# Performance work log

Measured on AMD Instinct MI355X. Metric: run time of the kernel, lower is better.

## Reference

```python
import jax, jax.numpy as jnp
import numpy as np

N = 50000          # nodes
E = 800000         # edges (avg degree 16)
NFEAT = 128        # dim_touched / gcn_nfeat
NHID = 96
NCLASS = 64
EXTRA = 32         # extra MLP-only features
NHID1, NHID2 = 128, 64
NN = 70            # top-k threshold rank
EPS = 1e-5         # BatchNorm1d eps


def setup_inputs() -> dict:
    key = jax.random.key(0)
    ks = jax.random.split(key, 24)
    x = jax.random.normal(ks[0], (N, NFEAT + EXTRA + 1), jnp.float32)
    grp = jax.random.randint(ks[1], (N,), 0, 2).astype(jnp.float32)
    x = x.at[:, -1].set(grp)  # last column is the group flag (target_group == 0)
    row = jax.random.randint(ks[2], (E,), 0, N, dtype=jnp.int32)
    col = jax.random.randint(ks[3], (E,), 0, N, dtype=jnp.int32)
    val = jax.random.uniform(ks[4], (E,), jnp.float32)

    def p(k, shape):
        return (jax.random.normal(k, shape, jnp.float32) * 0.05)

    return dict(
        x=x, row=row, col=col, val=val,
        W1=p(ks[5], (NFEAT, NHID)), b1=p(ks[6], (NHID,)),
        W2=p(ks[7], (NHID, NHID)), b2=p(ks[8], (NHID,)),
        W3=p(ks[9], (NHID, NHID)), b3=p(ks[10], (NHID,)),
        W4=p(ks[11], (NHID, NHID)), b4=p(ks[12], (NHID,)),
        W5=p(ks[13], (NHID, NCLASS)), b5=p(ks[14], (NCLASS,)),
        M1w=p(ks[15], (NCLASS + EXTRA, NHID1)), M1b=p(ks[16], (NHID1,)),
        M2w=p(ks[17], (NHID1, NHID2)), M2b=p(ks[18], (NHID2,)),
        M3w=p(ks[19], (NHID2, 1)), M3b=p(ks[20], (1,)),
    )


def _bn(h):
    # fresh BatchNorm1d in training mode, affine at default init (gamma=1, beta=0)
    m = jnp.mean(h, axis=0)
    v = jnp.mean((h - m) ** 2, axis=0)  # biased variance, as used for normalization
    return (h - m) * jax.lax.rsqrt(v + EPS)


def _gc(h, row, col, val, W, b):
    # GraphConvolution: spmm(adj, h @ W) + b, adj in COO form
    s = h @ W                                            # [N, out]
    msg = val[:, None] * s[col]                          # [E, out]
    agg = jax.ops.segment_sum(msg, row, num_segments=N)  # [N, out]
    return agg + b


def reference(x, row, col, val, W1, b1, W2, b2, W3, b3, W4, b4, W5, b5,
              M1w, M1b, M2w, M2b, M3w, M3b):
    h = x[:, :NFEAT]
    h = _bn(jax.nn.relu(_gc(h, row, col, val, W1, b1)))
    h = _bn(jax.nn.relu(_gc(h, row, col, val, W2, b2)))
    h = _bn(jax.nn.relu(_gc(h, row, col, val, W3, b3)))
    h = _bn(jax.nn.relu(_gc(h, row, col, val, W4, b4)))
    h = jax.nn.relu(_gc(h, row, col, val, W5, b5))        # [N, NCLASS]

    feat = jnp.concatenate([h, x[:, NFEAT:-1]], axis=1)   # [N, NCLASS+EXTRA]
    m = jax.nn.relu(feat @ M1w + M1b)
    m = jax.nn.relu(m @ M2w + M2b)
    m = m @ M3w + M3b                                     # [N, 1]

    # mask out target_group rows with the global min
    m = jnp.where(x[:, -1:] == 0.0, jnp.min(m), m)        # [N, 1]

    # top-70 threshold: value at descending rank NN
    thresh = jax.lax.top_k(m[:, 0], NN + 1)[0][NN]
    recip = jax.lax.stop_gradient(1.0 / m)                # torch reciprocal on detach()
    mask = jnp.where(m > thresh, recip, jnp.zeros_like(m))
    return m * mask
```

## Files before the change

### kernel.cpp

```cpp
#include <hip/hip_runtime.h>
#include <cstdint>
#include <cstddef>

#define XLD 161

typedef float f4u __attribute__((ext_vector_type(4), aligned(4)));
typedef float f4a __attribute__((ext_vector_type(4)));
typedef float f3u __attribute__((ext_vector_type(3), aligned(4)));

__global__ void hist_kernel(const int* __restrict__ row, int* __restrict__ cnt, int E) {
    for (int e = blockIdx.x * blockDim.x + threadIdx.x; e < E; e += gridDim.x * blockDim.x)
        atomicAdd(&cnt[row[e]], 1);
}

__global__ __launch_bounds__(256)
void scan1_kernel(const int* __restrict__ cnt, int* __restrict__ offs,
                  int* __restrict__ bsums, int n) {
    int t = threadIdx.x;
    int gid = blockIdx.x * 256 + t;
    int v = (gid < n) ? cnt[gid] : 0;
    int x = v;
#pragma unroll
    for (int o = 1; o < 64; o <<= 1) { int y = __shfl_up(x, o); if ((t & 63) >= o) x += y; }
    __shared__ int ws[4];
    if ((t & 63) == 63) ws[t >> 6] = x;
    __syncthreads();
    int add = 0;
    for (int w = 0; w < (t >> 6); w++) add += ws[w];
    int incl = x + add;
    if (gid < n) offs[gid] = incl - v;
    if (t == 255) bsums[blockIdx.x] = incl;
}

__global__ __launch_bounds__(256)
void scan2_kernel(int* __restrict__ bsums, int nb) {
    int t = threadIdx.x;
    int v = (t < nb) ? bsums[t] : 0;
    int x = v;
#pragma unroll
    for (int o = 1; o < 64; o <<= 1) { int y = __shfl_up(x, o); if ((t & 63) >= o) x += y; }
    __shared__ int ws[4];
    if ((t & 63) == 63) ws[t >> 6] = x;
    __syncthreads();
    int add = 0;
    for (int w = 0; w < (t >> 6); w++) add += ws[w];
    if (t < nb) bsums[t] = x + add - v;
}

__global__ void scan3_kernel(int* __restrict__ offs, int* __restrict__ cursor,
                             const int* __restrict__ bsums, int n, int E) {
    int gid = blockIdx.x * 256 + threadIdx.x;
    if (gid < n) {
        int o = offs[gid] + bsums[blockIdx.x];
        offs[gid] = o;
        cursor[gid] = o;
    }
    if (gid == 0) offs[n] = E;
}

__global__ void scatter_kernel(const int* __restrict__ row, const int* __restrict__ col,
                               const float* __restrict__ val, int* __restrict__ cursor,
                               int* __restrict__ colA, float* __restrict__ valA, int E) {
    for (int e = blockIdx.x * blockDim.x + threadIdx.x; e < E; e += gridDim.x * blockDim.x) {
        int r = row[e];
        int p = atomicAdd(&cursor[r], 1);
        colA[p] = col[e];
        valA[p] = val[e];
    }
}

template <int LC, bool WVS>
__global__ __launch_bounds__(256)
void aggP(const float* __restrict__ S, int ldS, const int* __restrict__ offs,
          const int* __restrict__ colA, const float* __restrict__ valA,
          float* __restrict__ Aout, float* __restrict__ vout, int n) {
    int lane = threadIdx.x & 63;
    int lg   = lane & 31;
    int grp  = threadIdx.x >> 5;
    int sh   = lane & 32;

    for (int node = blockIdx.x * 8 + grp; node < n; node += gridDim.x * 8) {
        int e0 = offs[node], e1 = offs[node + 1];
        float acc[LC];
#pragma unroll
        for (int a = 0; a < LC; a++) acc[a] = 0.f;
        float vsum = 0.f;

        for (int e = e0; e < e1; e += 32) {
            int   idx = e + lg;
            int   ce = (idx < e1) ? colA[idx] : 0;
            float ve = (idx < e1) ? valA[idx] : 0.f;
            int   cnt = min(32, e1 - e);
#pragma unroll 8
            for (int j = 0; j < cnt; j++) {
                int   c = __shfl(ce, sh + j);
                float v = __shfl(ve, sh + j);
                const float* srow = S + (size_t)c * ldS + LC * lg;
                if (LC == 3) {
                    f3u g = *(const f3u*)srow;
                    acc[0] = fmaf(v, g[0], acc[0]);
                    acc[1] = fmaf(v, g[1], acc[1]);
                    acc[2] = fmaf(v, g[2], acc[2]);
                } else {
                    f4u g = *(const f4u*)srow;
                    acc[0] = fmaf(v, g[0], acc[0]);
                    acc[1] = fmaf(v, g[1], acc[1]);
                    acc[2] = fmaf(v, g[2], acc[2]);
                    acc[3] = fmaf(v, g[3], acc[3]);
                }
                vsum += v;
            }
        }

        float* orow = Aout + (size_t)node * (32 * LC) + LC * lg;
        if (LC == 3) {
            f3u o; o[0] = acc[0]; o[1] = acc[1]; o[2] = acc[2];
            *(f3u*)orow = o;
        } else {
            f4u o; o[0] = acc[0]; o[1] = acc[1]; o[2] = acc[2]; o[3] = acc[3];
            *(f4u*)orow = o;
        }
        if (WVS && lg == 0) vout[node] = vsum;
    }
}

template <int CT>
__device__ inline void ldw(const float* p, float* wv) {
    if constexpr (CT == 4) { *(f4a*)wv = *(const f4a*)p; }
    else if constexpr (CT == 6) { *(f3u*)wv = *(const f3u*)p; *(f3u*)(wv + 3) = *(const f3u*)(p + 3); }
    else { *(f4a*)wv = *(const f4a*)p; *(f4a*)(wv + 4) = *(const f4a*)(p + 4); }
}

template <int K, int C, bool DOBN, bool HASCB>
__global__ __launch_bounds__(256)
void gemmF(const float* __restrict__ A1, int ld1, int split,
           const float* __restrict__ A2, int ld2,
           const float* __restrict__ W, const float* __restrict__ bias,
           const float* __restrict__ cbv, const float* __restrict__ vsum,
           float* __restrict__ Out, float* __restrict__ bsum,
           float* __restrict__ bsumsq, int n) {
    constexpr int CT = C / 16;
    __shared__ float Wc[16 * C];
    __shared__ float At[16][68];
    __shared__ float redS[DOBN ? C : 1];
    __shared__ float redQ[DOBN ? C : 1];

    int t  = threadIdx.x;
    int tc = t & 15, tr = t >> 4;
    int row0 = blockIdx.x * 64;

    if (DOBN && t < C) { redS[t] = 0.f; redQ[t] = 0.f; }

    int srow = t >> 2;
    int gr = row0 + srow; if (gr >= n) gr = n - 1;
    int kh = (t & 3) * 4;

    float acc[4][CT];
#pragma unroll
    for (int i = 0; i < 4; i++)
#pragma unroll
        for (int c = 0; c < CT; c++) acc[i][c] = 0.f;

    for (int kb = 0; kb < K; kb += 16) {
        __syncthreads();
        for (int i = t * 4; i < 16 * C; i += 1024)
            *(f4a*)&Wc[i] = *(const f4u*)&W[(size_t)kb * C + i];
        {
            int kg = kb + kh;
            const float* src = (kg < split) ? (A1 + (size_t)gr * ld1 + kg)
                                            : (A2 + (size_t)gr * ld2 + (kg - split));
            f4u v = *(const f4u*)src;
#pragma unroll
            for (int e = 0; e < 4; e++) At[kh + e][srow] = v[e];
        }
        __syncthreads();
#pragma unroll
        for (int kk = 0; kk < 16; kk++) {
            f4a av = *(const f4a*)&At[kk][tr * 4];
            float wv[CT];
            ldw<CT>(&Wc[kk * C + tc * CT], wv);
#pragma unroll
            for (int i = 0; i < 4; i++)
#pragma unroll
                for (int c = 0; c < CT; c++) acc[i][c] = fmaf(av[i], wv[c], acc[i][c]);
        }
    }

    float bb[CT], cc[CT];
#pragma unroll
    for (int c = 0; c < CT; c++) {
        bb[c] = bias[tc * CT + c];
        cc[c] = HASCB ? cbv[tc * CT + c] : 0.f;
    }
    float ps[CT], pq[CT];
#pragma unroll
    for (int c = 0; c < CT; c++) { ps[c] = 0.f; pq[c] = 0.f; }

#pragma unroll
    for (int i = 0; i < 4; i++) {
        int r = row0 + tr * 4 + i;
        if (r < n) {
            float vs = HASCB ? vsum[r] : 0.f;
            float* o = Out + (size_t)r * C + tc * CT;
#pragma unroll
            for (int c = 0; c < CT; c++) {
                float v = acc[i][c] + vs * cc[c] + bb[c];
                v = fmaxf(v, 0.f);
                o[c] = v;
                if (DOBN) { ps[c] += v; pq[c] += v * v; }
            }
        }
    }
    if (DOBN) {
#pragma unroll
        for (int c = 0; c < CT; c++) {
            ps[c] += __shfl_xor(ps[c], 16);
            ps[c] += __shfl_xor(ps[c], 32);
            pq[c] += __shfl_xor(pq[c], 16);
            pq[c] += __shfl_xor(pq[c], 32);
        }
        if ((t & 48) == 0) {
#pragma unroll
            for (int c = 0; c < CT; c++) {
                atomicAdd(&redS[tc * CT + c], ps[c]);
                atomicAdd(&redQ[tc * CT + c], pq[c]);
            }
        }
        __syncthreads();
        if (t < C) {
            atomicAdd(&bsum[t], redS[t]);
            atomicAdd(&bsumsq[t], redQ[t]);
        }
    }
}

template <int C>
__global__ __launch_bounds__(256)
void fold_kernel(const float* __restrict__ W, float* __restrict__ bsum,
                 float* __restrict__ bsumsq, float* __restrict__ Wf,
                 float* __restrict__ cb, int N) {
    __shared__ float mean[96], inv[96];
    int t = threadIdx.x;
    float rn = 1.0f / (float)N;
    if (t < 96) {
        float mu  = bsum[t] * rn;
        float var = bsumsq[t] * rn - mu * mu;
        mean[t] = mu;
        inv[t]  = rsqrtf(var + 1e-5f);
        bsum[t] = 0.f;
        bsumsq[t] = 0.f;
    }
    __syncthreads();
    for (int i = t; i < 96 * C; i += 256) {
        int k = i / C;
        Wf[i] = inv[k] * W[i];
    }
    if (t < C) {
        float s = 0.f;
        for (int k = 0; k < 96; k++) s += mean[k] * inv[k] * W[k * C + t];
        cb[t] = -s;
    }
}

__global__ __launch_bounds__(256)
void dot_min_kernel(const float* __restrict__ A, const float* __restrict__ M3w,
                    const float* __restrict__ M3b, float* __restrict__ m,
                    unsigned* __restrict__ gmin, int n) {
    int lane = threadIdx.x & 63;
    int wv   = threadIdx.x >> 6;
    float w  = M3w[lane];
    float b  = M3b[0];
    float lmin = 3.4e38f;
    int nw = gridDim.x * 4;
    for (int r = blockIdx.x * 4 + wv; r < n; r += nw) {
        float v = A[(size_t)r * 64 + lane] * w;
#pragma unroll
        for (int o = 32; o; o >>= 1) v += __shfl_down(v, o);
        if (lane == 0) {
            float mv = v + b;
            m[r] = mv;
            lmin = fminf(lmin, mv);
        }
    }
#pragma unroll
    for (int o = 32; o; o >>= 1) lmin = fminf(lmin, __shfl_down(lmin, o));
    __shared__ float sm[4];
    if (lane == 0) sm[wv] = lmin;
    __syncthreads();
    if (threadIdx.x == 0) {
        float mn = fminf(fminf(sm[0], sm[1]), fminf(sm[2], sm[3]));
        unsigned u = __float_as_uint(mn);
        unsigned key = (u >> 31) ? ~u : (u | 0x80000000u);
        atomicMin(gmin, key);
    }
}

__global__ void where_kernel(const float* __restrict__ x, float* __restrict__ m,
                             const unsigned* __restrict__ gmin, int n) {
    int i = blockIdx.x * blockDim.x + threadIdx.x;
    if (i < n) {
        unsigned k = *gmin;
        unsigned u = (k >> 31) ? (k ^ 0x80000000u) : ~k;
        float g = __uint_as_float(u);
        if (x[(size_t)i * XLD + 160] == 0.0f) m[i] = g;
    }
}

__device__ inline unsigned fkey(float f) {
    unsigned u = __float_as_uint(f);
    return (u >> 31) ? ~u : (u | 0x80000000u);
}

__global__ __launch_bounds__(1024)
void select_kernel(const float* __restrict__ m, int n, int kwant, float* __restrict__ thresh) {
    __shared__ unsigned hist[256];
    __shared__ unsigned sprefix;
    __shared__ int skk;
    int t = threadIdx.x;
    if (t == 0) { sprefix = 0u; skk = kwant; }
    for (int pass = 0; pass < 4; ++pass) {
        if (t < 256) hist[t] = 0u;
        __syncthreads();
        int shift = 24 - 8 * pass;
        unsigned pfx = sprefix;
        for (int i = t; i < n; i += 1024) {
            unsigned key = fkey(m[i]);
            bool ok = (pass == 0) || ((key >> (shift + 8)) == (pfx >> (shift + 8)));
            if (ok) atomicAdd(&hist[(key >> shift) & 255u], 1u);
        }
        __syncthreads();
        if (t == 0) {
            int cum = 0, kk = skk, chosen = 0;
            for (int b = 255; b >= 0; b--) {
                cum += (int)hist[b];
                if (cum >= kk) { chosen = b; kk -= (cum - (int)hist[b]); break; }
            }
            sprefix = pfx | ((unsigned)chosen << shift);
            skk = kk;
        }
        __syncthreads();
    }
    if (t == 0) {
        unsigned key = sprefix;
        unsigned u = (key >> 31) ? (key ^ 0x80000000u) : ~key;
        *thresh = __uint_as_float(u);
    }
}

__global__ void mask_kernel(const float* __restrict__ m, const float* __restrict__ thresh,
                            float* __restrict__ out, int n) {
    int i = blockIdx.x * blockDim.x + threadIdx.x;
    if (i < n) {
        float t = *thresh, v = m[i];
        out[i] = (v > t) ? v * (1.0f / v) : 0.0f;
    }
}

extern "C" void kernel_launch(void* const* d_in, const int* in_sizes, int n_in,
                              void* d_out, int out_size, void* d_ws, size_t ws_size,
                              hipStream_t stream) {
    const float* x   = (const float*)d_in[0];
    const int*   row = (const int*)d_in[1];
    const int*   col = (const int*)d_in[2];
    const float* val = (const float*)d_in[3];
    const float* W1  = (const float*)d_in[4];
    const float* b1  = (const float*)d_in[5];
    const float* W2  = (const float*)d_in[6];
    const float* b2  = (const float*)d_in[7];
    const float* W3  = (const float*)d_in[8];
    const float* b3  = (const float*)d_in[9];
    const float* W4  = (const float*)d_in[10];
    const float* b4  = (const float*)d_in[11];
    const float* W5  = (const float*)d_in[12];
    const float* b5  = (const float*)d_in[13];
    const float* M1w = (const float*)d_in[14];
    const float* M1b = (const float*)d_in[15];
    const float* M2w = (const float*)d_in[16];
    const float* M2b = (const float*)d_in[17];
    const float* M3w = (const float*)d_in[18];
    const float* M3b = (const float*)d_in[19];

    const int n = in_sizes[0] / XLD;
    const int E = in_sizes[1];

    char* ws = (char*)d_ws;
    size_t off = 0;
    auto carve = [&](size_t bytes) -> void* {
        void* p = ws + off;
        off = (off + bytes + 255) & ~(size_t)255;
        return p;
    };
    int*      offs   = (int*)carve((size_t)(n + 1) * 4);
    int*      cursor = (int*)carve((size_t)n * 4);
    int*      bsums  = (int*)carve(256 * 4);
    int*      colA   = (int*)carve((size_t)E * 4);
    float*    valA   = (float*)carve((size_t)E * 4);
    float*    h      = (float*)carve((size_t)n * 96 * 4);
    float*    big    = (float*)carve((size_t)n * 128 * 4);
    float*    Wf     = (float*)carve(96 * 96 * 4);
    float*    stats  = (float*)carve(192 * 4);
    float*    cb     = (float*)carve(96 * 4);
    float*    vsum   = (float*)carve((size_t)n * 4);
    float*    m      = (float*)carve((size_t)n * 4);
    unsigned* gmin   = (unsigned*)carve(4);
    float*    thresh = (float*)carve(4);
    float* bsum   = stats;
    float* bsumsq = stats + 96;

    hipMemsetAsync(cursor, 0, (size_t)n * 4, stream);
    hipMemsetAsync(stats, 0, 192 * 4, stream);
    hipMemsetAsync(gmin, 0xFF, 4, stream);

    const int nb = (n + 255) / 256;
    hist_kernel<<<512, 256, 0, stream>>>(row, cursor, E);
    scan1_kernel<<<nb, 256, 0, stream>>>(cursor, offs, bsums, n);
    scan2_kernel<<<1, 256, 0, stream>>>(bsums, nb);
    scan3_kernel<<<nb, 256, 0, stream>>>(offs, cursor, bsums, n, E);
    scatter_kernel<<<512, 256, 0, stream>>>(row, col, val, cursor, colA, valA, E);

    const int gB = (n + 63) / 64;
    const int ga = 3072;

    aggP<4, true><<<ga, 256, 0, stream>>>(x, XLD, offs, colA, valA, big, vsum, n);
    gemmF<128, 96, true, false><<<gB, 256, 0, stream>>>(big, 128, 128, big, 128,
        W1, b1, nullptr, nullptr, h, bsum, bsumsq, n);

    fold_kernel<96><<<1, 256, 0, stream>>>(W2, bsum, bsumsq, Wf, cb, n);
    aggP<3, false><<<ga, 256, 0, stream>>>(h, 96, offs, colA, valA, big, nullptr, n);
    gemmF<96, 96, true, true><<<gB, 256, 0, stream>>>(big, 96, 96, big, 96,
        Wf, b2, cb, vsum, h, bsum, bsumsq, n);

    fold_kernel<96><<<1, 256, 0, stream>>>(W3, bsum, bsumsq, Wf, cb, n);
    aggP<3, false><<<ga, 256, 0, stream>>>(h, 96, offs, colA, valA, big, nullptr, n);
    gemmF<96, 96, true, true><<<gB, 256, 0, stream>>>(big, 96, 96, big, 96,
        Wf, b3, cb, vsum, h, bsum, bsumsq, n);

    fold_kernel<96><<<1, 256, 0, stream>>>(W4, bsum, bsumsq, Wf, cb, n);
    aggP<3, false><<<ga, 256, 0, stream>>>(h, 96, offs, colA, valA, big, nullptr, n);
    gemmF<96, 96, true, true><<<gB, 256, 0, stream>>>(big, 96, 96, big, 96,
        Wf, b4, cb, vsum, h, bsum, bsumsq, n);

    fold_kernel<64><<<1, 256, 0, stream>>>(W5, bsum, bsumsq, Wf, cb, n);
    aggP<3, false><<<ga, 256, 0, stream>>>(h, 96, offs, colA, valA, big, nullptr, n);
    gemmF<96, 64, false, true><<<gB, 256, 0, stream>>>(big, 96, 96, big, 96,
        Wf, b5, cb, vsum, h, bsum, bsumsq, n);

    gemmF<96, 128, false, false><<<gB, 256, 0, stream>>>(h, 64, 64, x + 128, XLD,
        M1w, M1b, nullptr, nullptr, big, bsum, bsumsq, n);
    gemmF<128, 64, false, false><<<gB, 256, 0, stream>>>(big, 128, 128, big, 128,
        M2w, M2b, nullptr, nullptr, h, bsum, bsumsq, n);

    dot_min_kernel<<<256, 256, 0, stream>>>(h, M3w, M3b, m, gmin, n);

    where_kernel<<<(n + 255) / 256, 256, 0, stream>>>(x, m, gmin, n);

    select_kernel<<<1, 1024, 0, stream>>>(m, n, 71, thresh);

    mask_kernel<<<(n + 255) / 256, 256, 0, stream>>>(m, thresh, (float*)d_out, n);
}
```

Before: 824.2 us.

## Aggregate with one thread per node and feature slice, pack edges as int2

The SpMM aggregation moves from a half-wavefront per node, with shuffles broadcasting each edge, to one thread per node per feature slice. The grid is split into 8 slices of 16 or 12 columns, and each thread loads whole row slices with float4 reads and processes two edges at a time for memory-level parallelism. Column index and value are packed into one int2 array so each edge is a single 8-byte load. The cost is uncoalesced per-thread row gathers and load imbalance across threads in a wavefront when node degrees differ.

```diff
diff --git a/kernel.cpp b/kernel.cpp
--- a/kernel.cpp
+++ b/kernel.cpp
@@ -60,68 +60,77 @@
 
 __global__ void scatter_kernel(const int* __restrict__ row, const int* __restrict__ col,
                                const float* __restrict__ val, int* __restrict__ cursor,
-                               int* __restrict__ colA, float* __restrict__ valA, int E) {
+                               int2* __restrict__ edges, int E) {
     for (int e = blockIdx.x * blockDim.x + threadIdx.x; e < E; e += gridDim.x * blockDim.x) {
         int r = row[e];
         int p = atomicAdd(&cursor[r], 1);
-        colA[p] = col[e];
-        valA[p] = val[e];
-    }
-}
-
-template <int LC, bool WVS>
-__global__ __launch_bounds__(256)
-void aggP(const float* __restrict__ S, int ldS, const int* __restrict__ offs,
-          const int* __restrict__ colA, const float* __restrict__ valA,
-          float* __restrict__ Aout, float* __restrict__ vout, int n) {
-    int lane = threadIdx.x & 63;
-    int lg   = lane & 31;
-    int grp  = threadIdx.x >> 5;
-    int sh   = lane & 32;
-
-    for (int node = blockIdx.x * 8 + grp; node < n; node += gridDim.x * 8) {
-        int e0 = offs[node], e1 = offs[node + 1];
-        float acc[LC];
-#pragma unroll
-        for (int a = 0; a < LC; a++) acc[a] = 0.f;
-        float vsum = 0.f;
-
-        for (int e = e0; e < e1; e += 32) {
-            int   idx = e + lg;
-            int   ce = (idx < e1) ? colA[idx] : 0;
-            float ve = (idx < e1) ? valA[idx] : 0.f;
-            int   cnt = min(32, e1 - e);
-#pragma unroll 8
-            for (int j = 0; j < cnt; j++) {
-                int   c = __shfl(ce, sh + j);
-                float v = __shfl(ve, sh + j);
-                const float* srow = S + (size_t)c * ldS + LC * lg;
-                if (LC == 3) {
-                    f3u g = *(const f3u*)srow;
-                    acc[0] = fmaf(v, g[0], acc[0]);
-                    acc[1] = fmaf(v, g[1], acc[1]);
-                    acc[2] = fmaf(v, g[2], acc[2]);
-                } else {
-                    f4u g = *(const f4u*)srow;
-                    acc[0] = fmaf(v, g[0], acc[0]);
-                    acc[1] = fmaf(v, g[1], acc[1]);
-                    acc[2] = fmaf(v, g[2], acc[2]);
-                    acc[3] = fmaf(v, g[3], acc[3]);
-                }
-                vsum += v;
+        int2 ed;
+        ed.x = col[e];
+        ed.y = __float_as_int(val[e]);
+        edges[p] = ed;
+    }
+}
+
+template <int F, bool WVS>
+__global__ __launch_bounds__(256)
+void aggS(const float* __restrict__ S, int ldS, const int* __restrict__ offs,
+          const int2* __restrict__ edges, float* __restrict__ Aout, int ldO,
+          float* __restrict__ vout, int n) {
+    int slice = blockIdx.x & 7;
+    int node  = (blockIdx.x >> 3) * 256 + threadIdx.x;
+    if (node >= n) return;
+    int soff = slice * F;
+    int e0 = offs[node], e1 = offs[node + 1];
+
+    float acc[F];
+#pragma unroll
+    for (int a = 0; a < F; a++) acc[a] = 0.f;
+    float vsum = 0.f;
+
+    int e = e0;
+    for (; e + 2 <= e1; e += 2) {
+        int2 ea = edges[e];
+        int2 eb = edges[e + 1];
+        const float* sa = S + (size_t)ea.x * ldS + soff;
+        const float* sb = S + (size_t)eb.x * ldS + soff;
+        float va = __int_as_float(ea.y);
+        float vb = __int_as_float(eb.y);
+        f4u ga[F / 4], gb[F / 4];
+#pragma unroll
+        for (int q = 0; q < F / 4; q++) ga[q] = *(const f4u*)(sa + 4 * q);
+#pragma unroll
+        for (int q = 0; q < F / 4; q++) gb[q] = *(const f4u*)(sb + 4 * q);
+#pragma unroll
+        for (int q = 0; q < F / 4; q++)
+#pragma unroll
+            for (int z = 0; z < 4; z++) {
+                acc[4 * q + z] = fmaf(va, ga[q][z], acc[4 * q + z]);
+                acc[4 * q + z] = fmaf(vb, gb[q][z], acc[4 * q + z]);
             }
-        }
-
-        float* orow = Aout + (size_t)node * (32 * LC) + LC * lg;
-        if (LC == 3) {
-            f3u o; o[0] = acc[0]; o[1] = acc[1]; o[2] = acc[2];
-            *(f3u*)orow = o;
-        } else {
-            f4u o; o[0] = acc[0]; o[1] = acc[1]; o[2] = acc[2]; o[3] = acc[3];
-            *(f4u*)orow = o;
-        }
-        if (WVS && lg == 0) vout[node] = vsum;
-    }
+        vsum += va + vb;
+    }
+    if (e < e1) {
+        int2 ea = edges[e];
+        const float* sa = S + (size_t)ea.x * ldS + soff;
+        float va = __int_as_float(ea.y);
+#pragma unroll
+        for (int q = 0; q < F / 4; q++) {
+            f4u g = *(const f4u*)(sa + 4 * q);
+#pragma unroll
+            for (int z = 0; z < 4; z++) acc[4 * q + z] = fmaf(va, g[z], acc[4 * q + z]);
+        }
+        vsum += va;
+    }
+
+    float* o = Aout + (size_t)node * ldO + soff;
+#pragma unroll
+    for (int q = 0; q < F / 4; q++) {
+        f4u v;
+#pragma unroll
+        for (int z = 0; z < 4; z++) v[z] = acc[4 * q + z];
+        *(f4u*)(o + 4 * q) = v;
+    }
+    if (WVS && slice == 0) vout[node] = vsum;
 }
 
 template <int CT>
@@ -393,8 +402,7 @@
     int*      offs   = (int*)carve((size_t)(n + 1) * 4);
     int*      cursor = (int*)carve((size_t)n * 4);
     int*      bsums  = (int*)carve(256 * 4);
-    int*      colA   = (int*)carve((size_t)E * 4);
-    float*    valA   = (float*)carve((size_t)E * 4);
+    int2*     edges  = (int2*)carve((size_t)E * 8);
     float*    h      = (float*)carve((size_t)n * 96 * 4);
     float*    big    = (float*)carve((size_t)n * 128 * 4);
     float*    Wf     = (float*)carve(96 * 96 * 4);
@@ -416,32 +424,32 @@
     scan1_kernel<<<nb, 256, 0, stream>>>(cursor, offs, bsums, n);
     scan2_kernel<<<1, 256, 0, stream>>>(bsums, nb);
     scan3_kernel<<<nb, 256, 0, stream>>>(offs, cursor, bsums, n, E);
-    scatter_kernel<<<512, 256, 0, stream>>>(row, col, val, cursor, colA, valA, E);
+    scatter_kernel<<<512, 256, 0, stream>>>(row, col, val, cursor, edges, E);
 
     const int gB = (n + 63) / 64;
-    const int ga = 3072;
-
-    aggP<4, true><<<ga, 256, 0, stream>>>(x, XLD, offs, colA, valA, big, vsum, n);
+    const int gS = nb * 8;
+
+    aggS<16, true><<<gS, 256, 0, stream>>>(x, XLD, offs, edges, big, 128, vsum, n);
     gemmF<128, 96, true, false><<<gB, 256, 0, stream>>>(big, 128, 128, big, 128,
         W1, b1, nullptr, nullptr, h, bsum, bsumsq, n);
 
     fold_kernel<96><<<1, 256, 0, stream>>>(W2, bsum, bsumsq, Wf, cb, n);
-    aggP<3, false><<<ga, 256, 0, stream>>>(h, 96, offs, colA, valA, big, nullptr, n);
+    aggS<12, false><<<gS, 256, 0, stream>>>(h, 96, offs, edges, big, 96, nullptr, n);
     gemmF<96, 96, true, true><<<gB, 256, 0, stream>>>(big, 96, 96, big, 96,
         Wf, b2, cb, vsum, h, bsum, bsumsq, n);
 
     fold_kernel<96><<<1, 256, 0, stream>>>(W3, bsum, bsumsq, Wf, cb, n);
-    aggP<3, false><<<ga, 256, 0, stream>>>(h, 96, offs, colA, valA, big, nullptr, n);
+    aggS<12, false><<<gS, 256, 0, stream>>>(h, 96, offs, edges, big, 96, nullptr, n);
     gemmF<96, 96, true, true><<<gB, 256, 0, stream>>>(big, 96, 96, big, 96,
         Wf, b3, cb, vsum, h, bsum, bsumsq, n);
 
     fold_kernel<96><<<1, 256, 0, stream>>>(W4, bsum, bsumsq, Wf, cb, n);
-    aggP<3, false><<<ga, 256, 0, stream>>>(h, 96, offs, colA, valA, big, nullptr, n);
+    aggS<12, false><<<gS, 256, 0, stream>>>(h, 96, offs, edges, big, 96, nullptr, n);
     gemmF<96, 96, true, true><<<gB, 256, 0, stream>>>(big, 96, 96, big, 96,
         Wf, b4, cb, vsum, h, bsum, bsumsq, n);
 
     fold_kernel<64><<<1, 256, 0, stream>>>(W5, bsum, bsumsq, Wf, cb, n);
-    aggP<3, false><<<ga, 256, 0, stream>>>(h, 96, offs, colA, valA, big, nullptr, n);
+    aggS<12, false><<<gS, 256, 0, stream>>>(h, 96, offs, edges, big, 96, nullptr, n);
     gemmF<96, 64, false, true><<<gB, 256, 0, stream>>>(big, 96, 96, big, 96,
         Wf, b5, cb, vsum, h, bsum, bsumsq, n);
 
```

After: 1.529 ms. 1.85x slower.

## Reorder GCN layers to transform-then-aggregate and fuse bias/ReLU/BN stats into gather

Applied to the files above, without the earlier changes.

Each graph convolution now runs the dense GEMM first, with the BatchNorm shift folded in as a per-column constant, and then aggregates over edges. The bias, ReLU and BatchNorm sum and sum-of-squares are computed in the aggregation epilogue, so the per-node val-sum buffer and the GEMM-side reductions go away. In layer 1 the gather now reads 96-wide rows instead of 128-wide ones. Edge column and value are packed into a single int2 array to halve index loads, and the GEMMs are split across two column blocks to give more parallelism. The cost is a per-block shared-memory reduction for the statistics inside the gather kernel and more GEMM blocks that each reload their A tiles.

```diff
diff --git a/kernel.cpp b/kernel.cpp
--- a/kernel.cpp
+++ b/kernel.cpp
@@ -7,6 +7,7 @@
 typedef float f4u __attribute__((ext_vector_type(4), aligned(4)));
 typedef float f4a __attribute__((ext_vector_type(4)));
 typedef float f3u __attribute__((ext_vector_type(3), aligned(4)));
+typedef float f2a __attribute__((ext_vector_type(2)));
 
 __global__ void hist_kernel(const int* __restrict__ row, int* __restrict__ cnt, int E) {
     for (int e = blockIdx.x * blockDim.x + threadIdx.x; e < E; e += gridDim.x * blockDim.x)
@@ -60,176 +61,188 @@
 
 __global__ void scatter_kernel(const int* __restrict__ row, const int* __restrict__ col,
                                const float* __restrict__ val, int* __restrict__ cursor,
-                               int* __restrict__ colA, float* __restrict__ valA, int E) {
+                               int2* __restrict__ edges, int E) {
     for (int e = blockIdx.x * blockDim.x + threadIdx.x; e < E; e += gridDim.x * blockDim.x) {
         int r = row[e];
         int p = atomicAdd(&cursor[r], 1);
-        colA[p] = col[e];
-        valA[p] = val[e];
-    }
-}
-
-template <int LC, bool WVS>
-__global__ __launch_bounds__(256)
-void aggP(const float* __restrict__ S, int ldS, const int* __restrict__ offs,
-          const int* __restrict__ colA, const float* __restrict__ valA,
-          float* __restrict__ Aout, float* __restrict__ vout, int n) {
+        int2 ed;
+        ed.x = col[e];
+        ed.y = __float_as_int(val[e]);
+        edges[p] = ed;
+    }
+}
+
+template <int CT>
+__device__ inline void ldw(const float* p, float* wv) {
+    if constexpr (CT == 2) { *(f2a*)wv = *(const f2a*)p; }
+    else if constexpr (CT == 3) { *(f3u*)wv = *(const f3u*)p; }
+    else { *(f4a*)wv = *(const f4a*)p; }
+}
+
+template <int K, int COLS, bool HASB, bool RELU, bool HASCB>
+__global__ __launch_bounds__(256)
+void gemmC(const float* __restrict__ A1, int ld1, int split,
+           const float* __restrict__ A2, int ld2,
+           const float* __restrict__ W, int ldW,
+           const float* __restrict__ bias, const float* __restrict__ cbv,
+           float* __restrict__ Out, int ldO, int n) {
+    constexpr int CT = COLS / 16;
+    __shared__ float Wc[16 * COLS];
+    __shared__ float At[16][68];
+
+    int t  = threadIdx.x;
+    int tc = t & 15, tr = t >> 4;
+    int row0 = blockIdx.x * 64;
+    int col0 = blockIdx.y * COLS;
+
+    int srow = t >> 2;
+    int gr = row0 + srow; if (gr >= n) gr = n - 1;
+    int kh = (t & 3) * 4;
+
+    float acc[4][CT];
+#pragma unroll
+    for (int i = 0; i < 4; i++)
+#pragma unroll
+        for (int c = 0; c < CT; c++) acc[i][c] = 0.f;
+
+#pragma unroll 1
+    for (int kb = 0; kb < K; kb += 16) {
+        __syncthreads();
+        for (int i4 = t * 4; i4 < 16 * COLS; i4 += 1024) {
+            int k = i4 / COLS, j = i4 - k * COLS;
+            *(f4a*)&Wc[i4] = *(const f4u*)&W[(size_t)(kb + k) * ldW + col0 + j];
+        }
+        {
+            int kg = kb + kh;
+            const float* src = (kg < split) ? (A1 + (size_t)gr * ld1 + kg)
+                                            : (A2 + (size_t)gr * ld2 + (kg - split));
+            f4u v = *(const f4u*)src;
+#pragma unroll
+            for (int e = 0; e < 4; e++) At[kh + e][srow] = v[e];
+        }
+        __syncthreads();
+#pragma unroll
+        for (int kk = 0; kk < 16; kk++) {
+            f4a av = *(const f4a*)&At[kk][tr * 4];
+            float wv[CT];
+            ldw<CT>(&Wc[kk * COLS + tc * CT], wv);
+#pragma unroll
+            for (int i = 0; i < 4; i++)
+#pragma unroll
+                for (int c = 0; c < CT; c++) acc[i][c] = fmaf(av[i], wv[c], acc[i][c]);
+        }
+    }
+
+    float bb[CT], cc[CT];
+#pragma unroll
+    for (int c = 0; c < CT; c++) {
+        bb[c] = HASB ? bias[col0 + tc * CT + c] : 0.f;
+        cc[c] = HASCB ? cbv[col0 + tc * CT + c] : 0.f;
+    }
+
+#pragma unroll
+    for (int i = 0; i < 4; i++) {
+        int r = row0 + tr * 4 + i;
+        if (r < n) {
+            float* o = Out + (size_t)r * ldO + col0 + tc * CT;
+#pragma unroll
+            for (int c = 0; c < CT; c++) {
+                float v = acc[i][c] + cc[c] + bb[c];
+                if (RELU) v = fmaxf(v, 0.f);
+                o[c] = v;
+            }
+        }
+    }
+}
+
+template <int LC, bool DOBN>
+__global__ __launch_bounds__(256)
+void aggE(const float* __restrict__ S, const int* __restrict__ offs,
+          const int2* __restrict__ edges, const float* __restrict__ bias,
+          float* __restrict__ Hout, float* __restrict__ bsum,
+          float* __restrict__ bsumsq, int n) {
+    constexpr int C = 32 * LC;
     int lane = threadIdx.x & 63;
     int lg   = lane & 31;
     int grp  = threadIdx.x >> 5;
     int sh   = lane & 32;
 
+    float bir[LC];
+#pragma unroll
+    for (int a = 0; a < LC; a++) bir[a] = bias[LC * lg + a];
+
+    float psum[LC], psq[LC];
+#pragma unroll
+    for (int a = 0; a < LC; a++) { psum[a] = 0.f; psq[a] = 0.f; }
+
     for (int node = blockIdx.x * 8 + grp; node < n; node += gridDim.x * 8) {
         int e0 = offs[node], e1 = offs[node + 1];
         float acc[LC];
 #pragma unroll
         for (int a = 0; a < LC; a++) acc[a] = 0.f;
-        float vsum = 0.f;
 
         for (int e = e0; e < e1; e += 32) {
-            int   idx = e + lg;
-            int   ce = (idx < e1) ? colA[idx] : 0;
-            float ve = (idx < e1) ? valA[idx] : 0.f;
-            int   cnt = min(32, e1 - e);
+            int  idx = e + lg;
+            int2 ed  = (idx < e1) ? edges[idx] : make_int2(0, 0);
+            int  cnt = min(32, e1 - e);
 #pragma unroll 8
             for (int j = 0; j < cnt; j++) {
-                int   c = __shfl(ce, sh + j);
-                float v = __shfl(ve, sh + j);
-                const float* srow = S + (size_t)c * ldS + LC * lg;
+                int   c = __shfl(ed.x, sh + j);
+                float v = __int_as_float(__shfl(ed.y, sh + j));
+                const float* srow = S + (size_t)c * C + LC * lg;
                 if (LC == 3) {
                     f3u g = *(const f3u*)srow;
                     acc[0] = fmaf(v, g[0], acc[0]);
                     acc[1] = fmaf(v, g[1], acc[1]);
                     acc[2] = fmaf(v, g[2], acc[2]);
                 } else {
-                    f4u g = *(const f4u*)srow;
+                    f2a g = *(const f2a*)srow;
                     acc[0] = fmaf(v, g[0], acc[0]);
                     acc[1] = fmaf(v, g[1], acc[1]);
-                    acc[2] = fmaf(v, g[2], acc[2]);
-                    acc[3] = fmaf(v, g[3], acc[3]);
                 }
-                vsum += v;
             }
         }
 
-        float* orow = Aout + (size_t)node * (32 * LC) + LC * lg;
+        float* orow = Hout + (size_t)node * C + LC * lg;
         if (LC == 3) {
-            f3u o; o[0] = acc[0]; o[1] = acc[1]; o[2] = acc[2];
+            f3u o;
+#pragma unroll
+            for (int a = 0; a < 3; a++) {
+                float tv = fmaxf(acc[a] + bir[a], 0.f);
+                o[a] = tv;
+                if (DOBN) { psum[a] += tv; psq[a] += tv * tv; }
+            }
             *(f3u*)orow = o;
         } else {
-            f4u o; o[0] = acc[0]; o[1] = acc[1]; o[2] = acc[2]; o[3] = acc[3];
-            *(f4u*)orow = o;
-        }
-        if (WVS && lg == 0) vout[node] = vsum;
-    }
-}
-
-template <int CT>
-__device__ inline void ldw(const float* p, float* wv) {
-    if constexpr (CT == 4) { *(f4a*)wv = *(const f4a*)p; }
-    else if constexpr (CT == 6) { *(f3u*)wv = *(const f3u*)p; *(f3u*)(wv + 3) = *(const f3u*)(p + 3); }
-    else { *(f4a*)wv = *(const f4a*)p; *(f4a*)(wv + 4) = *(const f4a*)(p + 4); }
-}
-
-template <int K, int C, bool DOBN, bool HASCB>
-__global__ __launch_bounds__(256)
-void gemmF(const float* __restrict__ A1, int ld1, int split,
-           const float* __restrict__ A2, int ld2,
-           const float* __restrict__ W, const float* __restrict__ bias,
-           const float* __restrict__ cbv, const float* __restrict__ vsum,
-           float* __restrict__ Out, float* __restrict__ bsum,
-           float* __restrict__ bsumsq, int n) {
-    constexpr int CT = C / 16;
-    __shared__ float Wc[16 * C];
-    __shared__ float At[16][68];
-    __shared__ float redS[DOBN ? C : 1];
-    __shared__ float redQ[DOBN ? C : 1];
-
-    int t  = threadIdx.x;
-    int tc = t & 15, tr = t >> 4;
-    int row0 = blockIdx.x * 64;
-
-    if (DOBN && t < C) { redS[t] = 0.f; redQ[t] = 0.f; }
-
-    int srow = t >> 2;
-    int gr = row0 + srow; if (gr >= n) gr = n - 1;
-    int kh = (t & 3) * 4;
-
-    float acc[4][CT];
-#pragma unroll
-    for (int i = 0; i < 4; i++)
-#pragma unroll
-        for (int c = 0; c < CT; c++) acc[i][c] = 0.f;
-
-    for (int kb = 0; kb < K; kb += 16) {
-        __syncthreads();
-        for (int i = t * 4; i < 16 * C; i += 1024)
-            *(f4a*)&Wc[i] = *(const f4u*)&W[(size_t)kb * C + i];
-        {
-            int kg = kb + kh;
-            const float* src = (kg < split) ? (A1 + (size_t)gr * ld1 + kg)
-                                            : (A2 + (size_t)gr * ld2 + (kg - split));
-            f4u v = *(const f4u*)src;
-#pragma unroll
-            for (int e = 0; e < 4; e++) At[kh + e][srow] = v[e];
-        }
-        __syncthreads();
-#pragma unroll
-        for (int kk = 0; kk < 16; kk++) {
-            f4a av = *(const f4a*)&At[kk][tr * 4];
-            float wv[CT];
-            ldw<CT>(&Wc[kk * C + tc * CT], wv);
-#pragma unroll
-            for (int i = 0; i < 4; i++)
-#pragma unroll
-                for (int c = 0; c < CT; c++) acc[i][c] = fmaf(av[i], wv[c], acc[i][c]);
-        }
-    }
-
-    float bb[CT], cc[CT];
-#pragma unroll
-    for (int c = 0; c < CT; c++) {
-        bb[c] = bias[tc * CT + c];
-        cc[c] = HASCB ? cbv[tc * CT + c] : 0.f;
-    }
-    float ps[CT], pq[CT];
-#pragma unroll
-    for (int c = 0; c < CT; c++) { ps[c] = 0.f; pq[c] = 0.f; }
-
-#pragma unroll
-    for (int i = 0; i < 4; i++) {
-        int r = row0 + tr * 4 + i;
-        if (r < n) {
-            float vs = HASCB ? vsum[r] : 0.f;
-            float* o = Out + (size_t)r * C + tc * CT;
-#pragma unroll
-            for (int c = 0; c < CT; c++) {
-                float v = acc[i][c] + vs * cc[c] + bb[c];
-                v = fmaxf(v, 0.f);
-                o[c] = v;
-                if (DOBN) { ps[c] += v; pq[c] += v * v; }
+            f2a o;
+#pragma unroll
+            for (int a = 0; a < 2; a++) {
+                float tv = fmaxf(acc[a] + bir[a], 0.f);
+                o[a] = tv;
+                if (DOBN) { psum[a] += tv; psq[a] += tv * tv; }
             }
-        }
-    }
+            *(f2a*)orow = o;
+        }
+    }
+
     if (DOBN) {
-#pragma unroll
-        for (int c = 0; c < CT; c++) {
-            ps[c] += __shfl_xor(ps[c], 16);
-            ps[c] += __shfl_xor(ps[c], 32);
-            pq[c] += __shfl_xor(pq[c], 16);
-            pq[c] += __shfl_xor(pq[c], 32);
-        }
-        if ((t & 48) == 0) {
-#pragma unroll
-            for (int c = 0; c < CT; c++) {
-                atomicAdd(&redS[tc * CT + c], ps[c]);
-                atomicAdd(&redQ[tc * CT + c], pq[c]);
-            }
-        }
-        __syncthreads();
-        if (t < C) {
-            atomicAdd(&bsum[t], redS[t]);
-            atomicAdd(&bsumsq[t], redQ[t]);
+        __shared__ float red[DOBN ? 8 * C : 1];
+#pragma unroll
+        for (int a = 0; a < LC; a++) red[grp * C + LC * lg + a] = psum[a];
+        __syncthreads();
+        if (threadIdx.x < C) {
+            float s = 0.f;
+            for (int g = 0; g < 8; g++) s += red[g * C + threadIdx.x];
+            atomicAdd(&bsum[threadIdx.x], s);
+        }
+        __syncthreads();
+#pragma unroll
+        for (int a = 0; a < LC; a++) red[grp * C + LC * lg + a] = psq[a];
+        __syncthreads();
+        if (threadIdx.x < C) {
+            float s = 0.f;
+            for (int g = 0; g < 8; g++) s += red[g * C + threadIdx.x];
+            atomicAdd(&bsumsq[threadIdx.x], s);
         }
     }
 }
@@ -393,14 +406,12 @@
     int*      offs   = (int*)carve((size_t)(n + 1) * 4);
     int*      cursor = (int*)carve((size_t)n * 4);
     int*      bsums  = (int*)carve(256 * 4);
-    int*      colA   = (int*)carve((size_t)E * 4);
-    float*    valA   = (float*)carve((size_t)E * 4);
+    int2*     edges  = (int2*)carve((size_t)E * 8);
     float*    h      = (float*)carve((size_t)n * 96 * 4);
-    float*    big    = (float*)carve((size_t)n * 128 * 4);
+    float*    sbuf   = (float*)carve((size_t)n * 128 * 4);
     float*    Wf     = (float*)carve(96 * 96 * 4);
     float*    stats  = (float*)carve(192 * 4);
     float*    cb     = (float*)carve(96 * 4);
-    float*    vsum   = (float*)carve((size_t)n * 4);
     float*    m      = (float*)carve((size_t)n * 4);
     unsigned* gmin   = (unsigned*)carve(4);
     float*    thresh = (float*)carve(4);
@@ -416,39 +427,39 @@
     scan1_kernel<<<nb, 256, 0, stream>>>(cursor, offs, bsums, n);
     scan2_kernel<<<1, 256, 0, stream>>>(bsums, nb);
     scan3_kernel<<<nb, 256, 0, stream>>>(offs, cursor, bsums, n, E);
-    scatter_kernel<<<512, 256, 0, stream>>>(row, col, val, cursor, colA, valA, E);
-
-    const int gB = (n + 63) / 64;
-    const int ga = 3072;
-
-    aggP<4, true><<<ga, 256, 0, stream>>>(x, XLD, offs, colA, valA, big, vsum, n);
-    gemmF<128, 96, true, false><<<gB, 256, 0, stream>>>(big, 128, 128, big, 128,
-        W1, b1, nullptr, nullptr, h, bsum, bsumsq, n);
+    scatter_kernel<<<512, 256, 0, stream>>>(row, col, val, cursor, edges, E);
+
+    const int gR = (n + 63) / 64;
+    const int ga = 2048;
+
+    gemmC<128, 48, false, false, false><<<dim3(gR, 2), 256, 0, stream>>>(
+        x, XLD, 128, x, XLD, W1, 96, nullptr, nullptr, sbuf, 96, n);
+    aggE<3, true><<<ga, 256, 0, stream>>>(sbuf, offs, edges, b1, h, bsum, bsumsq, n);
 
     fold_kernel<96><<<1, 256, 0, stream>>>(W2, bsum, bsumsq, Wf, cb, n);
-    aggP<3, false><<<ga, 256, 0, stream>>>(h, 96, offs, colA, valA, big, nullptr, n);
-    gemmF<96, 96, true, true><<<gB, 256, 0, stream>>>(big, 96, 96, big, 96,
-        Wf, b2, cb, vsum, h, bsum, bsumsq, n);
+    gemmC<96, 48, false, false, true><<<dim3(gR, 2), 256, 0, stream>>>(
+        h, 96, 96, h, 96, Wf, 96, nullptr, cb, sbuf, 96, n);
+    aggE<3, true><<<ga, 256, 0, stream>>>(sbuf, offs, edges, b2, h, bsum, bsumsq, n);
 
     fold_kernel<96><<<1, 256, 0, stream>>>(W3, bsum, bsumsq, Wf, cb, n);
-    aggP<3, false><<<ga, 256, 0, stream>>>(h, 96, offs, colA, valA, big, nullptr, n);
-    gemmF<96, 96, true, true><<<gB, 256, 0, stream>>>(big, 96, 96, big, 96,
-        Wf, b3, cb, vsum, h, bsum, bsumsq, n);
+    gemmC<96, 48, false, false, true><<<dim3(gR, 2), 256, 0, stream>>>(
+        h, 96, 96, h, 96, Wf, 96, nullptr, cb, sbuf, 96, n);
+    aggE<3, true><<<ga, 256, 0, stream>>>(sbuf, offs, edges, b3, h, bsum, bsumsq, n);
 
     fold_kernel<96><<<1, 256, 0, stream>>>(W4, bsum, bsumsq, Wf, cb, n);
-    aggP<3, false><<<ga, 256, 0, stream>>>(h, 96, offs, colA, valA, big, nullptr, n);
-    gemmF<96, 96, true, true><<<gB, 256, 0, stream>>>(big, 96, 96, big, 96,
-        Wf, b4, cb, vsum, h, bsum, bsumsq, n);
+    gemmC<96, 48, false, false, true><<<dim3(gR, 2), 256, 0, stream>>>(
+        h, 96, 96, h, 96, Wf, 96, nullptr, cb, sbuf, 96, n);
+    aggE<3, true><<<ga, 256, 0, stream>>>(sbuf, offs, edges, b4, h, bsum, bsumsq, n);
 
     fold_kernel<64><<<1, 256, 0, stream>>>(W5, bsum, bsumsq, Wf, cb, n);
-    aggP<3, false><<<ga, 256, 0, stream>>>(h, 96, offs, colA, valA, big, nullptr, n);
-    gemmF<96, 64, false, true><<<gB, 256, 0, stream>>>(big, 96, 96, big, 96,
-        Wf, b5, cb, vsum, h, bsum, bsumsq, n);
-
-    gemmF<96, 128, false, false><<<gB, 256, 0, stream>>>(h, 64, 64, x + 128, XLD,
-        M1w, M1b, nullptr, nullptr, big, bsum, bsumsq, n);
-    gemmF<128, 64, false, false><<<gB, 256, 0, stream>>>(big, 128, 128, big, 128,
-        M2w, M2b, nullptr, nullptr, h, bsum, bsumsq, n);
+    gemmC<96, 32, false, false, true><<<dim3(gR, 2), 256, 0, stream>>>(
+        h, 96, 96, h, 96, Wf, 64, nullptr, cb, sbuf, 64, n);
+    aggE<2, false><<<ga, 256, 0, stream>>>(sbuf, offs, edges, b5, h, bsum, bsumsq, n);
+
+    gemmC<96, 64, true, true, false><<<dim3(gR, 2), 256, 0, stream>>>(
+        h, 64, 64, x + 128, XLD, M1w, 128, M1b, nullptr, sbuf, 128, n);
+    gemmC<128, 32, true, true, false><<<dim3(gR, 2), 256, 0, stream>>>(
+        sbuf, 128, 128, sbuf, 128, M2w, 64, M2b, nullptr, h, 64, n);
 
     dot_min_kernel<<<256, 256, 0, stream>>>(h, M3w, M3b, m, gmin, n);
 
```

New measurement: 882.5 us. +7.1%, slower.
